# Kernel optimization log

Hardware: AMD Instinct MI355X
Metric: run time of the kernel (lower is better)

## Reference

```python
import jax, jax.numpy as jnp
import numpy as np

RATIO = 0.08  # self.ratio_3 (frozen parameter)
# kernel point k -> (dx, dy) = (k//3-1, k%3-1); matches torch.meshgrid('ij') flattening in offset_modulation
GX = np.repeat(np.arange(-1, 2), 3)  # [-1,-1,-1,0,0,0,1,1,1]
GY = np.tile(np.arange(-1, 2), 3)    # [-1,0,1,-1,0,1,-1,0,1]


def conv3(x, w, b):
    y = jax.lax.conv_general_dilated(x, w, (1, 1), ((1, 1), (1, 1)),
                                     dimension_numbers=('NCHW', 'OIHW', 'NCHW'))
    return y + b[None, :, None, None]


def offset_modulation(offset):
    B, C, H, W = offset.shape
    ov = offset.reshape(B, C // 2, 2, H, W)
    crop = ov[:, 3:12]                      # 9 (x,y) pairs
    oxy = jnp.concatenate([crop[:, :, 0], crop[:, :, 1]], axis=1) * RATIO  # [B,18,H,W]
    grid = jnp.concatenate([jnp.asarray(GX), jnp.asarray(GY)]).astype(offset.dtype)
    return oxy - grid[None, :, None, None]


def bilinear_sample(x, py, px):
    # x: [B,C,H,W]; py,px: [B,H,W] float sample coords; zero outside bounds
    B, C, H, W = x.shape
    y0 = jnp.floor(py); x0 = jnp.floor(px)
    wy = py - y0; wx = px - x0
    def gather(yi, xi):
        valid = ((yi >= 0) & (yi < H) & (xi >= 0) & (xi < W)).astype(x.dtype)
        yc = jnp.clip(yi, 0, H - 1).astype(jnp.int32)
        xc = jnp.clip(xi, 0, W - 1).astype(jnp.int32)
        g = jax.vmap(lambda img, yy, xx: img[:, yy, xx])(x, yc, xc)  # [B,C,H,W]
        return g * valid[:, None]
    return (gather(y0, x0) * ((1 - wy) * (1 - wx))[:, None]
            + gather(y0, x0 + 1) * ((1 - wy) * wx)[:, None]
            + gather(y0 + 1, x0) * (wy * (1 - wx))[:, None]
            + gather(y0 + 1, x0 + 1) * (wy * wx)[:, None])


def deform_conv(x, off, w, b):
    # off: [B,18,H,W], channels 0..8 = dx per kernel point, 9..17 = dy
    B, C, H, W = x.shape
    by = jnp.arange(H, dtype=x.dtype)[None, :, None]
    bx = jnp.arange(W, dtype=x.dtype)[None, None, :]
    out = jnp.zeros((B, w.shape[0], H, W), x.dtype)
    for k in range(9):
        py = by + GY[k] + off[:, 9 + k]
        px = bx + GX[k] + off[:, k]
        s = bilinear_sample(x, py, px)
        out = out + jnp.einsum('bchw,oc->bohw', s, w[:, :, GY[k] + 1, GX[k] + 1])
    return out + b[None, :, None, None]


def setup_inputs():
    key = jax.random.key(0)
    ks = iter(jax.random.split(key, 32))
    def p(*shape):
        return jax.random.normal(next(ks), shape, jnp.float32) * 0.05
    inp = {
        'x': jax.random.normal(next(ks), (2, 64, 256, 256), jnp.float32),
        'offset_0': jax.random.normal(next(ks), (2, 24, 256, 256), jnp.float32),
        'l12_w': p(64, 64, 3, 3), 'l12_b': p(64),
        'l13_w1': p(64, 64, 3, 3), 'l13_b1': p(64),
        'l13_w2': p(64, 64, 3, 3), 'l13_b2': p(64),
        'l14_w1': p(64, 64, 3, 3), 'l14_b1': p(64),
        'l14_w2': p(64, 64, 3, 3), 'l14_b2': p(64),
        'l15_w': p(32, 64, 3, 3), 'l15_b': p(32),
        'd50_w': p(32, 32, 3, 3), 'd50_b': p(32),
        'd51_w': p(32, 32, 3, 3), 'd51_b': p(32),
        'd60_w': p(32, 32, 3, 3), 'd60_b': p(32),
        'd61_w': p(32, 32, 3, 3), 'd61_b': p(32),
        'l24_w': p(3, 32, 3, 3), 'l24_b': p(3),
    }
    return inp


def reference(x, offset_0, l12_w, l12_b, l13_w1, l13_b1, l13_w2, l13_b2,
              l14_w1, l14_b1, l14_w2, l14_b2, l15_w, l15_b,
              d50_w, d50_b, d51_w, d51_b, d60_w, d60_b, d61_w, d61_b,
              l24_w, l24_b):
    off = offset_modulation(offset_0)
    x = conv3(x, l12_w, l12_b)
    x = conv3(jax.nn.relu(conv3(x, l13_w1, l13_b1)), l13_w2, l13_b2) + x
    x = conv3(jax.nn.relu(conv3(x, l14_w1, l14_b1)), l14_w2, l14_b2) + x
    x = conv3(x, l15_w, l15_b)
    r5 = jax.nn.relu(deform_conv(x, off, d50_w, d50_b))
    r5 = deform_conv(r5, off, d51_w, d51_b)
    x = x + r5
    r6 = jax.nn.relu(deform_conv(x, off, d60_w, d60_b))
    r6 = deform_conv(r6, off, d61_w, d61_b)
    x = x + r6
    return conv3(x, l24_w, l24_b)
```

## Files before the change

### kernel.cpp

```cpp
#include <hip/hip_runtime.h>

#define HH 256
#define WW 256
#define HW (HH * WW)

typedef float f32x4 __attribute__((ext_vector_type(4)));
typedef short bf16x8 __attribute__((ext_vector_type(8)));

__device__ __forceinline__ unsigned short f2bf(float f) {
    union { float f; unsigned u; } v; v.f = f;
    unsigned r = v.u + 0x7fff + ((v.u >> 16) & 1);
    return (unsigned short)(r >> 16);
}
__device__ __forceinline__ float bflo(unsigned u) {
    union { unsigned u; float f; } v; v.u = u << 16; return v.f;
}
__device__ __forceinline__ float bfhi(unsigned u) {
    union { unsigned u; float f; } v; v.u = u & 0xffff0000u; return v.f;
}

__global__ void prepack_all(
    const float* w0, const float* w1, const float* w2, const float* w3,
    const float* w4, const float* w5, const float* w6, const float* w7,
    const float* w8, const float* w9,
    unsigned short* d0, unsigned short* d1, unsigned short* d2,
    unsigned short* d3, unsigned short* d4, unsigned short* d5,
    unsigned short* d6, unsigned short* d7, unsigned short* d8,
    unsigned short* d9) {
    const int L = blockIdx.y;
    const float* w; unsigned short* dst; int COUT, CIN;
    switch (L) {
        case 0: w = w0; dst = d0; COUT = 64; CIN = 64; break;
        case 1: w = w1; dst = d1; COUT = 64; CIN = 64; break;
        case 2: w = w2; dst = d2; COUT = 64; CIN = 64; break;
        case 3: w = w3; dst = d3; COUT = 64; CIN = 64; break;
        case 4: w = w4; dst = d4; COUT = 64; CIN = 64; break;
        case 5: w = w5; dst = d5; COUT = 32; CIN = 64; break;
        case 6: w = w6; dst = d6; COUT = 32; CIN = 32; break;
        case 7: w = w7; dst = d7; COUT = 32; CIN = 32; break;
        case 8: w = w8; dst = d8; COUT = 32; CIN = 32; break;
        default: w = w9; dst = d9; COUT = 32; CIN = 32; break;
    }
    int n = COUT * CIN * 9;
    int i = blockIdx.x * 256 + threadIdx.x;
    if (i >= n) return;
    int q = i & 31;
    int rest = i >> 5;
    int o = rest % COUT;
    int rest2 = rest / COUT;
    int KC = CIN >> 5;
    int kc = rest2 % KC;
    int t = rest2 / KC;
    int cin = kc * 32 + q;
    float v = w[((o * CIN + cin) * 3 + t / 3) * 3 + (t % 3)];
    dst[i] = f2bf(v);
}

template <bool SRCF32, int CIN, int COUT>
__global__ __launch_bounds__((COUT / 32) * 128) void convmfma(
    const void* __restrict__ in_, const unsigned short* __restrict__ wp,
    const float* __restrict__ bias, unsigned short* __restrict__ out) {
    constexpr int KC = CIN / 32;
    constexpr int WM = COUT / 32;
    constexpr int NT = WM * 128;
    constexpr int CSTR = 72;
    __shared__ unsigned short xt[204 * CSTR];

    const int tid = threadIdx.x;
    const int b = blockIdx.z;
    const int bx0 = blockIdx.x * 32;
    const int by0 = blockIdx.y * 4;

    if (SRCF32) {
        const float* inb = (const float*)in_ + (size_t)b * CIN * HW;
        for (int hp = tid; hp < 204; hp += NT) {
            int hy = hp / 34, hx = hp - hy * 34;
            int gy = by0 + hy - 1, gx = bx0 + hx - 1;
            bool ok = ((unsigned)gy < HH) && ((unsigned)gx < WW);
            const float* src = inb + ((size_t)gy * WW + gx);
            unsigned* dstp = (unsigned*)&xt[hp * CSTR];
#pragma unroll 4
            for (int c = 0; c < CIN; c += 2) {
                float v0 = ok ? src[(size_t)c * HW] : 0.f;
                float v1 = ok ? src[(size_t)(c + 1) * HW] : 0.f;
                dstp[c >> 1] = (unsigned)f2bf(v0) | ((unsigned)f2bf(v1) << 16);
            }
        }
    } else {
        const unsigned short* inb = (const unsigned short*)in_ + (size_t)b * HW * CIN;
        constexpr int CH = CIN / 8;
        for (int idx = tid; idx < 204 * CH; idx += NT) {
            int hp = idx / CH, sub = idx - hp * CH;
            int hy = hp / 34, hx = hp - hy * 34;
            int gy = by0 + hy - 1, gx = bx0 + hx - 1;
            uint4 v = {0, 0, 0, 0};
            if (((unsigned)gy < HH) && ((unsigned)gx < WW))
                v = *(const uint4*)&inb[((size_t)gy * WW + gx) * CIN + sub * 8];
            *(uint4*)&xt[hp * CSTR + sub * 8] = v;
        }
    }
    __syncthreads();

    const int lane = tid & 63;
    const int wv = tid >> 6;
    const int wm = (WM == 2) ? (wv & 1) : 0;
    const int wn = (WM == 2) ? (wv >> 1) : wv;
    const int l15 = lane & 15;
    const int kg = lane >> 4;

    f32x4 acc[2][4];
#pragma unroll
    for (int m = 0; m < 2; ++m)
#pragma unroll
        for (int n = 0; n < 4; ++n) acc[m][n] = {0.f, 0.f, 0.f, 0.f};

    int hbase[4];
#pragma unroll
    for (int n = 0; n < 4; ++n) {
        int p = wn * 64 + n * 16 + l15;
        hbase[n] = (p >> 5) * 34 + (p & 31);
    }

    const unsigned short* wlane = wp + ((size_t)(wm * 32 + l15) * 4 + kg) * 8;

#pragma unroll
    for (int t = 0; t < 9; ++t) {
        bf16x8 afr[2][KC];
#pragma unroll
        for (int kc = 0; kc < KC; ++kc)
#pragma unroll
            for (int m = 0; m < 2; ++m)
                afr[m][kc] = *(const bf16x8*)(wlane + ((size_t)(t * KC + kc) * COUT + m * 16) * 32);

        const int hoff = (t / 3) * 34 + (t % 3);
#pragma unroll
        for (int kc = 0; kc < KC; ++kc) {
            bf16x8 bfr[4];
#pragma unroll
            for (int n = 0; n < 4; ++n)
                bfr[n] = *(const bf16x8*)&xt[(hbase[n] + hoff) * CSTR + kc * 32 + kg * 8];
#pragma unroll
            for (int m = 0; m < 2; ++m)
#pragma unroll
                for (int n = 0; n < 4; ++n)
                    acc[m][n] = __builtin_amdgcn_mfma_f32_16x16x32_bf16(afr[m][kc], bfr[n], acc[m][n], 0, 0, 0);
        }
    }

    const size_t pixbase = (size_t)b * HW;
#pragma unroll
    for (int m = 0; m < 2; ++m) {
#pragma unroll
        for (int n = 0; n < 4; ++n) {
            int p = wn * 64 + n * 16 + l15;
            int gy = by0 + (p >> 5), gx = bx0 + (p & 31);
            size_t pidx = (pixbase + (size_t)gy * WW + gx) * COUT;
            int cb = wm * 32 + m * 16 + kg * 4;
            float v[4];
#pragma unroll
            for (int r = 0; r < 4; ++r) v[r] = acc[m][n][r] + bias[cb + r];
            uint2 o;
            o.x = (unsigned)f2bf(v[0]) | ((unsigned)f2bf(v[1]) << 16);
            o.y = (unsigned)f2bf(v[2]) | ((unsigned)f2bf(v[3]) << 16);
            *(uint2*)&out[pidx + cb] = o;
        }
    }
}

__global__ __launch_bounds__(256) void fusedres(
    const unsigned short* __restrict__ in, const unsigned short* __restrict__ w1p,
    const float* __restrict__ b1, const unsigned short* __restrict__ w2p,
    const float* __restrict__ b2, unsigned short* __restrict__ out) {
    constexpr int CS = 72;
    constexpr int MIDB = 160 * CS;
    __shared__ unsigned short xt[(160 + 128) * CS];

    const int tid = threadIdx.x;
    const int b = blockIdx.z;
    const int bx0 = blockIdx.x * 16;
    const int by0 = blockIdx.y * 4;

    const unsigned short* inb = in + (size_t)b * HW * 64;
    for (int idx = tid; idx < 160 * 8; idx += 256) {
        int hp = idx >> 3, sub = idx & 7;
        int hy = hp / 20, hx = hp - hy * 20;
        int gy = by0 + hy - 2, gx = bx0 + hx - 2;
        uint4 v = {0, 0, 0, 0};
        if (((unsigned)gy < HH) && ((unsigned)gx < WW))
            v = *(const uint4*)&inb[((size_t)gy * WW + gx) * 64 + sub * 8];
        *(uint4*)&xt[hp * CS + sub * 8] = v;
    }
    __syncthreads();

    const int lane = tid & 63;
    const int wv = tid >> 6;
    const int l15 = lane & 15;
    const int kg = lane >> 4;
    const int wm = wv & 1;
    const int gh = wv >> 1;

    f32x4 acc1[2][4];
#pragma unroll
    for (int m = 0; m < 2; ++m)
#pragma unroll
        for (int n = 0; n < 4; ++n) acc1[m][n] = {0.f, 0.f, 0.f, 0.f};

    int ib[4];
#pragma unroll
    for (int n = 0; n < 4; ++n) {
        int id = gh * 64 + n * 16 + l15;
        int rid = min(id, 107);
        int iy = rid / 18, ix = rid - iy * 18;
        ib[n] = iy * 20 + ix;
    }

    const unsigned short* w1l = w1p + ((size_t)(wm * 32 + l15) * 4 + kg) * 8;
#pragma unroll
    for (int t = 0; t < 9; ++t) {
        bf16x8 afr[2][2];
#pragma unroll
        for (int kc = 0; kc < 2; ++kc)
#pragma unroll
            for (int m = 0; m < 2; ++m)
                afr[kc][m] = *(const bf16x8*)(w1l + ((size_t)(t * 2 + kc) * 64 + m * 16) * 32);
        const int hoff = (t / 3) * 20 + (t % 3);
#pragma unroll
        for (int kc = 0; kc < 2; ++kc) {
            bf16x8 bfr[4];
#pragma unroll
            for (int n = 0; n < 4; ++n)
                bfr[n] = *(const bf16x8*)&xt[(ib[n] + hoff) * CS + kc * 32 + kg * 8];
#pragma unroll
            for (int m = 0; m < 2; ++m)
#pragma unroll
                for (int n = 0; n < 4; ++n)
                    acc1[m][n] = __builtin_amdgcn_mfma_f32_16x16x32_bf16(afr[kc][m], bfr[n], acc1[m][n], 0, 0, 0);
        }
    }
#pragma unroll
    for (int n = 0; n < 4; ++n) {
        int id = gh * 64 + n * 16 + l15;
        int rid = min(id, 107);
        int iy = rid / 18, ix = rid - iy * 18;
        int gy = by0 - 1 + iy, gx = bx0 - 1 + ix;
        bool ok = ((unsigned)gy < HH) && ((unsigned)gx < WW) && (id < 108);
#pragma unroll
        for (int m = 0; m < 2; ++m) {
            int cb = wm * 32 + m * 16 + kg * 4;
            float v[4];
#pragma unroll
            for (int r = 0; r < 4; ++r)
                v[r] = ok ? fmaxf(acc1[m][n][r] + b1[cb + r], 0.f) : 0.f;
            uint2 o;
            o.x = (unsigned)f2bf(v[0]) | ((unsigned)f2bf(v[1]) << 16);
            o.y = (unsigned)f2bf(v[2]) | ((unsigned)f2bf(v[3]) << 16);
            *(uint2*)&xt[MIDB + id * CS + cb] = o;
        }
    }
    __syncthreads();

    f32x4 acc2[2][2];
#pragma unroll
    for (int m = 0; m < 2; ++m)
#pragma unroll
        for (int n = 0; n < 2; ++n) acc2[m][n] = {0.f, 0.f, 0.f, 0.f};

    int mb[2];
#pragma unroll
    for (int n = 0; n < 2; ++n) {
        int p = gh * 32 + n * 16 + l15;
        mb[n] = (p >> 4) * 18 + (p & 15);
    }
    const unsigned short* w2l = w2p + ((size_t)(wm * 32 + l15) * 4 + kg) * 8;
#pragma unroll
    for (int t = 0; t < 9; ++t) {
        bf16x8 afr[2][2];
#pragma unroll
        for (int kc = 0; kc < 2; ++kc)
#pragma unroll
            for (int m = 0; m < 2; ++m)
                afr[kc][m] = *(const bf16x8*)(w2l + ((size_t)(t * 2 + kc) * 64 + m * 16) * 32);
        const int hoff = (t / 3) * 18 + (t % 3);
#pragma unroll
        for (int kc = 0; kc < 2; ++kc) {
            bf16x8 bfr[2];
#pragma unroll
            for (int n = 0; n < 2; ++n)
                bfr[n] = *(const bf16x8*)&xt[MIDB + (mb[n] + hoff) * CS + kc * 32 + kg * 8];
#pragma unroll
            for (int m = 0; m < 2; ++m)
#pragma unroll
                for (int n = 0; n < 2; ++n)
                    acc2[m][n] = __builtin_amdgcn_mfma_f32_16x16x32_bf16(afr[kc][m], bfr[n], acc2[m][n], 0, 0, 0);
        }
    }

    unsigned short* outb = out + (size_t)b * HW * 64;
#pragma unroll
    for (int n = 0; n < 2; ++n) {
        int p = gh * 32 + n * 16 + l15;
        int oy = p >> 4, ox = p & 15;
        int gy = by0 + oy, gx = bx0 + ox;
        int rs = (oy + 2) * 20 + ox + 2;
        size_t pidx = ((size_t)gy * WW + gx) * 64;
#pragma unroll
        for (int m = 0; m < 2; ++m) {
            int cb = wm * 32 + m * 16 + kg * 4;
            float v[4];
#pragma unroll
            for (int r = 0; r < 4; ++r) v[r] = acc2[m][n][r] + b2[cb + r];
            uint2 rr = *(const uint2*)&xt[rs * CS + cb];
            v[0] += bflo(rr.x); v[1] += bfhi(rr.x);
            v[2] += bflo(rr.y); v[3] += bfhi(rr.y);
            uint2 o;
            o.x = (unsigned)f2bf(v[0]) | ((unsigned)f2bf(v[1]) << 16);
            o.y = (unsigned)f2bf(v[2]) | ((unsigned)f2bf(v[3]) << 16);
            *(uint2*)&outb[pidx + cb] = o;
        }
    }
}

__global__ __launch_bounds__(512) void dpair(
    const unsigned short* __restrict__ in, const float* __restrict__ off0,
    const unsigned short* __restrict__ w1p, const float* __restrict__ b1,
    const unsigned short* __restrict__ w2p, const float* __restrict__ b2,
    unsigned short* __restrict__ out) {
    constexpr int CS = 40;
    constexpr int MIDB = 432 * CS;
    __shared__ unsigned short xt[(432 + 352) * CS];

    const int tid = threadIdx.x;
    const int b = blockIdx.z;
    const int bx0 = blockIdx.x * 32;
    const int by0 = blockIdx.y * 8;

    const unsigned short* inb = in + (size_t)b * HW * 32;
    for (int idx = tid; idx < 432 * 4; idx += 512) {
        int hp = idx >> 2, sub = idx & 3;
        int hy = hp / 36, hx = hp - hy * 36;
        int gy = by0 + hy - 2, gx = bx0 + hx - 2;
        uint4 v = {0, 0, 0, 0};
        if (((unsigned)gy < HH) && ((unsigned)gx < WW))
            v = *(const uint4*)&inb[((size_t)gy * WW + gx) * 32 + sub * 8];
        *(uint4*)&xt[hp * CS + sub * 8] = v;
    }
    __syncthreads();

    const int lane = tid & 63;
    const int wv = tid >> 6;
    const int l15 = lane & 15;
    const int kg = lane >> 4;
    const float* offB = off0 + (size_t)b * 24 * HW;

    f32x4 acc1[2][3];
#pragma unroll
    for (int m = 0; m < 2; ++m)
#pragma unroll
        for (int f = 0; f < 3; ++f) acc1[m][f] = {0.f, 0.f, 0.f, 0.f};

    int fgy[3], fgx[3], foff[3];
#pragma unroll
    for (int f = 0; f < 3; ++f) {
        int id = (wv * 3 + f) * 16 + l15;
        int rid = min(id, 339);
        int iy = rid / 34, ix = rid - iy * 34;
        fgy[f] = by0 - 1 + iy;
        fgx[f] = bx0 - 1 + ix;
        int cy = min(max(fgy[f], 0), HH - 1);
        int cx = min(max(fgx[f], 0), WW - 1);
        foff[f] = cy * WW + cx;
    }
    const unsigned short* w1l = w1p + (size_t)(l15 * 32 + kg * 8);

#pragma unroll 1
    for (int t = 0; t < 9; ++t) {
        const int k = (t % 3) * 3 + t / 3;
        const float* offx = offB + (size_t)(6 + 2 * k) * HW;
        const float* offy = offB + (size_t)(7 + 2 * k) * HW;
        bf16x8 afr[2];
#pragma unroll
        for (int m = 0; m < 2; ++m)
            afr[m] = *(const bf16x8*)(w1l + (size_t)(t * 32 + m * 16) * 32);

        bf16x8 bfr[3];
#pragma unroll
        for (int f = 0; f < 3; ++f) {
            float dxv = offx[foff[f]] * 0.08f;
            float dyv = offy[foff[f]] * 0.08f;
            float pxf = (float)fgx[f] + dxv;
            float pyf = (float)fgy[f] + dyv;
            float x0f = floorf(pxf), y0f = floorf(pyf);
            float wx = pxf - x0f, wy = pyf - y0f;
            int tx0 = min(max((int)x0f - (bx0 - 2), 0), 34);
            int ty0 = min(max((int)y0f - (by0 - 2), 0), 10);
            int lp = ty0 * 36 + tx0;
            uint4 a00 = *(const uint4*)&xt[lp * CS + kg * 8];
            uint4 a01 = *(const uint4*)&xt[(lp + 1) * CS + kg * 8];
            uint4 a10 = *(const uint4*)&xt[(lp + 36) * CS + kg * 8];
            uint4 a11 = *(const uint4*)&xt[(lp + 37) * CS + kg * 8];
            float w00 = (1.f - wy) * (1.f - wx), w01 = (1.f - wy) * wx;
            float w10 = wy * (1.f - wx), w11 = wy * wx;
            unsigned c00[4] = {a00.x, a00.y, a00.z, a00.w};
            unsigned c01[4] = {a01.x, a01.y, a01.z, a01.w};
            unsigned c10[4] = {a10.x, a10.y, a10.z, a10.w};
            unsigned c11[4] = {a11.x, a11.y, a11.z, a11.w};
            union { bf16x8 v; unsigned u[4]; } ur;
#pragma unroll
            for (int j = 0; j < 4; ++j) {
                float slo = w00 * bflo(c00[j]) + w01 * bflo(c01[j]) +
                            w10 * bflo(c10[j]) + w11 * bflo(c11[j]);
                float shi = w00 * bfhi(c00[j]) + w01 * bfhi(c01[j]) +
                            w10 * bfhi(c10[j]) + w11 * bfhi(c11[j]);
                ur.u[j] = (unsigned)f2bf(slo) | ((unsigned)f2bf(shi) << 16);
            }
            bfr[f] = ur.v;
        }
#pragma unroll
        for (int m = 0; m < 2; ++m)
#pragma unroll
            for (int f = 0; f < 3; ++f)
                acc1[m][f] = __builtin_amdgcn_mfma_f32_16x16x32_bf16(afr[m], bfr[f], acc1[m][f], 0, 0, 0);
    }
#pragma unroll
    for (int f = 0; f < 3; ++f) {
        int id = (wv * 3 + f) * 16 + l15;
        bool ok = ((unsigned)fgy[f] < HH) && ((unsigned)fgx[f] < WW) && (id < 340);
        int wid = min(id, 351);
#pragma unroll
        for (int m = 0; m < 2; ++m) {
            int cb = m * 16 + kg * 4;
            float v[4];
#pragma unroll
            for (int r = 0; r < 4; ++r)
                v[r] = ok ? fmaxf(acc1[m][f][r] + b1[cb + r], 0.f) : 0.f;
            uint2 o;
            o.x = (unsigned)f2bf(v[0]) | ((unsigned)f2bf(v[1]) << 16);
            o.y = (unsigned)f2bf(v[2]) | ((unsigned)f2bf(v[3]) << 16);
            *(uint2*)&xt[MIDB + wid * CS + cb] = o;
        }
    }
    __syncthreads();

    f32x4 acc2[2][2];
#pragma unroll
    for (int m = 0; m < 2; ++m)
#pragma unroll
        for (int n = 0; n < 2; ++n) acc2[m][n] = {0.f, 0.f, 0.f, 0.f};

    const int py = by0 + wv;
    const unsigned short* w2l = w2p + (size_t)(l15 * 32 + kg * 8);

#pragma unroll 1
    for (int t = 0; t < 9; ++t) {
        const int k = (t % 3) * 3 + t / 3;
        const float* offx = offB + (size_t)(6 + 2 * k) * HW + (size_t)py * WW;
        const float* offy = offB + (size_t)(7 + 2 * k) * HW + (size_t)py * WW;
        bf16x8 afr[2];
#pragma unroll
        for (int m = 0; m < 2; ++m)
            afr[m] = *(const bf16x8*)(w2l + (size_t)(t * 32 + m * 16) * 32);

        bf16x8 bfr[2];
#pragma unroll
        for (int n = 0; n < 2; ++n) {
            const int pxi = bx0 + n * 16 + l15;
            float dxv = offx[pxi] * 0.08f;
            float dyv = offy[pxi] * 0.08f;
            float pxf = (float)pxi + dxv;
            float pyf = (float)py + dyv;
            float x0f = floorf(pxf), y0f = floorf(pyf);
            float wx = pxf - x0f, wy = pyf - y0f;
            int mx0 = min(max((int)x0f - (bx0 - 1), 0), 32);
            int my0 = min(max((int)y0f - (by0 - 1), 0), 8);
            int lp = my0 * 34 + mx0;
            uint4 a00 = *(const uint4*)&xt[MIDB + lp * CS + kg * 8];
            uint4 a01 = *(const uint4*)&xt[MIDB + (lp + 1) * CS + kg * 8];
            uint4 a10 = *(const uint4*)&xt[MIDB + (lp + 34) * CS + kg * 8];
            uint4 a11 = *(const uint4*)&xt[MIDB + (lp + 35) * CS + kg * 8];
            float w00 = (1.f - wy) * (1.f - wx), w01 = (1.f - wy) * wx;
            float w10 = wy * (1.f - wx), w11 = wy * wx;
            unsigned c00[4] = {a00.x, a00.y, a00.z, a00.w};
            unsigned c01[4] = {a01.x, a01.y, a01.z, a01.w};
            unsigned c10[4] = {a10.x, a10.y, a10.z, a10.w};
            unsigned c11[4] = {a11.x, a11.y, a11.z, a11.w};
            union { bf16x8 v; unsigned u[4]; } ur;
#pragma unroll
            for (int j = 0; j < 4; ++j) {
                float slo = w00 * bflo(c00[j]) + w01 * bflo(c01[j]) +
                            w10 * bflo(c10[j]) + w11 * bflo(c11[j]);
                float shi = w00 * bfhi(c00[j]) + w01 * bfhi(c01[j]) +
                            w10 * bfhi(c10[j]) + w11 * bfhi(c11[j]);
                ur.u[j] = (unsigned)f2bf(slo) | ((unsigned)f2bf(shi) << 16);
            }
            bfr[n] = ur.v;
        }
#pragma unroll
        for (int m = 0; m < 2; ++m)
#pragma unroll
            for (int n = 0; n < 2; ++n)
                acc2[m][n] = __builtin_amdgcn_mfma_f32_16x16x32_bf16(afr[m], bfr[n], acc2[m][n], 0, 0, 0);
    }

    unsigned short* outb = out + (size_t)b * HW * 32;
#pragma unroll
    for (int n = 0; n < 2; ++n) {
        int gx = bx0 + n * 16 + l15;
        int rs = (wv + 2) * 36 + (n * 16 + l15) + 2;
        size_t pidx = ((size_t)py * WW + gx) * 32;
#pragma unroll
        for (int m = 0; m < 2; ++m) {
            int cb = m * 16 + kg * 4;
            float v[4];
#pragma unroll
            for (int r = 0; r < 4; ++r) v[r] = acc2[m][n][r] + b2[cb + r];
            uint2 rr = *(const uint2*)&xt[rs * CS + cb];
            v[0] += bflo(rr.x); v[1] += bfhi(rr.x);
            v[2] += bflo(rr.y); v[3] += bfhi(rr.y);
            uint2 o;
            o.x = (unsigned)f2bf(v[0]) | ((unsigned)f2bf(v[1]) << 16);
            o.y = (unsigned)f2bf(v[2]) | ((unsigned)f2bf(v[3]) << 16);
            *(uint2*)&outb[pidx + cb] = o;
        }
    }
}

__global__ __launch_bounds__(256) void conv3f(const unsigned short* __restrict__ in,
                                              const float* __restrict__ wgt,
                                              const float* __restrict__ bias,
                                              float* __restrict__ out) {
    __shared__ unsigned short xt[324 * 34];
    const int tid = threadIdx.x;
    const int lx = tid & 15, ly = tid >> 4;
    const int bx = blockIdx.x << 4, by = blockIdx.y << 4;
    const int b = blockIdx.z;

    const unsigned short* inb = in + (size_t)b * HW * 32;
    for (int idx = tid; idx < 324 * 8; idx += 256) {
        int hp = idx >> 3, sub = idx & 7;
        int hy = hp / 18, hx = hp - hy * 18;
        int gy = by + hy - 1, gx = bx + hx - 1;
        uint2 v = {0, 0};
        if (((unsigned)gy < HH) && ((unsigned)gx < WW))
            v = *(const uint2*)&inb[((size_t)gy * WW + gx) * 32 + sub * 4];
        *(uint2*)&xt[hp * 34 + sub * 4] = v;
    }
    __syncthreads();

    float a0 = bias[0], a1 = bias[1], a2 = bias[2];
#pragma unroll
    for (int ty = 0; ty < 3; ++ty) {
#pragma unroll
        for (int tx = 0; tx < 3; ++tx) {
            const unsigned short* row = &xt[((ly + ty) * 18 + lx + tx) * 34];
#pragma unroll 8
            for (int c = 0; c < 32; c += 2) {
                unsigned pv = *(const unsigned*)&row[c];
                float vl = bflo(pv), vh = bfhi(pv);
                const float* wl = wgt + (size_t)(c * 3 + ty) * 3 + tx;
                const float* whp = wgt + (size_t)((c + 1) * 3 + ty) * 3 + tx;
                a0 = fmaf(vl, wl[0], a0);          a0 = fmaf(vh, whp[0], a0);
                a1 = fmaf(vl, wl[32 * 9], a1);     a1 = fmaf(vh, whp[32 * 9], a1);
                a2 = fmaf(vl, wl[64 * 9], a2);     a2 = fmaf(vh, whp[64 * 9], a2);
            }
        }
    }
    const size_t o0 = ((size_t)b * 3) * HW + (size_t)(by + ly) * WW + bx + lx;
    out[o0] = a0;
    out[o0 + HW] = a1;
    out[o0 + 2 * HW] = a2;
}

extern "C" void kernel_launch(void* const* d_in, const int* in_sizes, int n_in,
                              void* d_out, int out_size, void* d_ws, size_t ws_size,
                              hipStream_t stream) {
    const float* x    = (const float*)d_in[0];
    const float* off0 = (const float*)d_in[1];
    const float* w12  = (const float*)d_in[2];
    const float* b12  = (const float*)d_in[3];
    const float* w13a = (const float*)d_in[4];
    const float* b13a = (const float*)d_in[5];
    const float* w13b = (const float*)d_in[6];
    const float* b13b = (const float*)d_in[7];
    const float* w14a = (const float*)d_in[8];
    const float* b14a = (const float*)d_in[9];
    const float* w14b = (const float*)d_in[10];
    const float* b14b = (const float*)d_in[11];
    const float* w15  = (const float*)d_in[12];
    const float* b15  = (const float*)d_in[13];
    const float* w50  = (const float*)d_in[14];
    const float* b50  = (const float*)d_in[15];
    const float* w51  = (const float*)d_in[16];
    const float* b51  = (const float*)d_in[17];
    const float* w60  = (const float*)d_in[18];
    const float* b60  = (const float*)d_in[19];
    const float* w61  = (const float*)d_in[20];
    const float* b61  = (const float*)d_in[21];
    const float* w24  = (const float*)d_in[22];
    const float* b24  = (const float*)d_in[23];

    unsigned short* A  = (unsigned short*)d_ws;
    unsigned short* Bb = A + (size_t)2 * HW * 64;
    unsigned short* D  = Bb;
    unsigned short* E  = Bb + (size_t)2 * HW * 32;
    unsigned short* wpk = Bb + (size_t)2 * HW * 64;
    const int SZ64 = 64 * 64 * 9;
    const int SZ32 = 32 * 64 * 9;
    const int SZD  = 32 * 32 * 9;
    unsigned short* p12  = wpk;
    unsigned short* p13a = p12 + SZ64;
    unsigned short* p13b = p13a + SZ64;
    unsigned short* p14a = p13b + SZ64;
    unsigned short* p14b = p14a + SZ64;
    unsigned short* p15  = p14b + SZ64;
    unsigned short* q50  = p15 + SZ32;
    unsigned short* q51  = q50 + SZD;
    unsigned short* q60  = q51 + SZD;
    unsigned short* q61  = q60 + SZD;
    float* out = (float*)d_out;

    prepack_all<<<dim3(144, 10), 256, 0, stream>>>(
        w12, w13a, w13b, w14a, w14b, w15, w50, w51, w60, w61,
        p12, p13a, p13b, p14a, p14b, p15, q50, q51, q60, q61);

    dim3 gm(WW / 32, HH / 4, 2);
    dim3 gf(WW / 16, HH / 4, 2);
    dim3 gd(WW / 32, HH / 8, 2);
    dim3 gs(HH / 16, WW / 16, 2);

    convmfma<true, 64, 64><<<gm, 256, 0, stream>>>(x, p12, b12, A);
    fusedres<<<gf, 256, 0, stream>>>(A,  p13a, b13a, p13b, b13b, Bb);
    fusedres<<<gf, 256, 0, stream>>>(Bb, p14a, b14a, p14b, b14b, A);
    convmfma<false, 64, 32><<<gm, 128, 0, stream>>>(A, p15, b15, D);
    dpair<<<gd, 512, 0, stream>>>(D, off0, q50, b50, q51, b51, E);
    dpair<<<gd, 512, 0, stream>>>(E, off0, q60, b60, q61, b61, D);
    conv3f<<<gs, 256, 0, stream>>>(D, w24, b24, out);
}
```

Before: 251.5 us.

## Replace fused residual-block kernels with separate larger-tile conv launches

Removes the fusedres kernel, which computed both convs of each residual block with a recomputed halo for the intermediate. Each residual block now runs as two convmfma launches with ReLU and residual-add epilogue template flags. convmfma is retiled so each 256-thread block covers an 8x32 pixel tile and each wave computes all output channels for its 2 rows, which increases weight reuse per block. The change removes the halo recompute but adds an extra round trip of the intermediate activation through global memory and two more launches. It also reads and writes A in place in the residual step, which is safe only because each pixel is read and written by the same thread.

```diff
diff --git a/kernel.cpp b/kernel.cpp
--- a/kernel.cpp
+++ b/kernel.cpp
@@ -56,24 +56,24 @@
     dst[i] = f2bf(v);
 }
 
-template <bool SRCF32, int CIN, int COUT>
-__global__ __launch_bounds__((COUT / 32) * 128) void convmfma(
+template <bool SRCF32, int CIN, int COUT, bool RELU, bool ADDRES>
+__global__ __launch_bounds__(256) void convmfma(
     const void* __restrict__ in_, const unsigned short* __restrict__ wp,
-    const float* __restrict__ bias, unsigned short* __restrict__ out) {
+    const float* __restrict__ bias, const unsigned short* __restrict__ res,
+    unsigned short* __restrict__ out) {
     constexpr int KC = CIN / 32;
-    constexpr int WM = COUT / 32;
-    constexpr int NT = WM * 128;
+    constexpr int WM = COUT / 16;
     constexpr int CSTR = 72;
-    __shared__ unsigned short xt[204 * CSTR];
+    __shared__ unsigned short xt[340 * CSTR];
 
     const int tid = threadIdx.x;
     const int b = blockIdx.z;
     const int bx0 = blockIdx.x * 32;
-    const int by0 = blockIdx.y * 4;
+    const int by0 = blockIdx.y * 8;
 
     if (SRCF32) {
         const float* inb = (const float*)in_ + (size_t)b * CIN * HW;
-        for (int hp = tid; hp < 204; hp += NT) {
+        for (int hp = tid; hp < 340; hp += 256) {
             int hy = hp / 34, hx = hp - hy * 34;
             int gy = by0 + hy - 1, gx = bx0 + hx - 1;
             bool ok = ((unsigned)gy < HH) && ((unsigned)gx < WW);
@@ -89,7 +89,7 @@
     } else {
         const unsigned short* inb = (const unsigned short*)in_ + (size_t)b * HW * CIN;
         constexpr int CH = CIN / 8;
-        for (int idx = tid; idx < 204 * CH; idx += NT) {
+        for (int idx = tid; idx < 340 * CH; idx += 256) {
             int hp = idx / CH, sub = idx - hp * CH;
             int hy = hp / 34, hx = hp - hy * 34;
             int gy = by0 + hy - 1, gx = bx0 + hx - 1;
@@ -103,33 +103,31 @@
 
     const int lane = tid & 63;
     const int wv = tid >> 6;
-    const int wm = (WM == 2) ? (wv & 1) : 0;
-    const int wn = (WM == 2) ? (wv >> 1) : wv;
     const int l15 = lane & 15;
     const int kg = lane >> 4;
 
-    f32x4 acc[2][4];
-#pragma unroll
-    for (int m = 0; m < 2; ++m)
+    f32x4 acc[WM][4];
+#pragma unroll
+    for (int m = 0; m < WM; ++m)
 #pragma unroll
         for (int n = 0; n < 4; ++n) acc[m][n] = {0.f, 0.f, 0.f, 0.f};
 
     int hbase[4];
 #pragma unroll
     for (int n = 0; n < 4; ++n) {
-        int p = wn * 64 + n * 16 + l15;
-        hbase[n] = (p >> 5) * 34 + (p & 31);
-    }
-
-    const unsigned short* wlane = wp + ((size_t)(wm * 32 + l15) * 4 + kg) * 8;
+        int p = n * 16 + l15;
+        hbase[n] = (2 * wv + (p >> 5)) * 34 + (p & 31);
+    }
+
+    const unsigned short* wlane = wp + ((size_t)l15 * 4 + kg) * 8;
 
 #pragma unroll
     for (int t = 0; t < 9; ++t) {
-        bf16x8 afr[2][KC];
+        bf16x8 afr[WM][KC];
 #pragma unroll
         for (int kc = 0; kc < KC; ++kc)
 #pragma unroll
-            for (int m = 0; m < 2; ++m)
+            for (int m = 0; m < WM; ++m)
                 afr[m][kc] = *(const bf16x8*)(wlane + ((size_t)(t * KC + kc) * COUT + m * 16) * 32);
 
         const int hoff = (t / 3) * 34 + (t % 3);
@@ -140,7 +138,7 @@
             for (int n = 0; n < 4; ++n)
                 bfr[n] = *(const bf16x8*)&xt[(hbase[n] + hoff) * CSTR + kc * 32 + kg * 8];
 #pragma unroll
-            for (int m = 0; m < 2; ++m)
+            for (int m = 0; m < WM; ++m)
 #pragma unroll
                 for (int n = 0; n < 4; ++n)
                     acc[m][n] = __builtin_amdgcn_mfma_f32_16x16x32_bf16(afr[m][kc], bfr[n], acc[m][n], 0, 0, 0);
@@ -149,173 +147,28 @@
 
     const size_t pixbase = (size_t)b * HW;
 #pragma unroll
-    for (int m = 0; m < 2; ++m) {
-#pragma unroll
-        for (int n = 0; n < 4; ++n) {
-            int p = wn * 64 + n * 16 + l15;
-            int gy = by0 + (p >> 5), gx = bx0 + (p & 31);
-            size_t pidx = (pixbase + (size_t)gy * WW + gx) * COUT;
-            int cb = wm * 32 + m * 16 + kg * 4;
+    for (int n = 0; n < 4; ++n) {
+        int p = n * 16 + l15;
+        int gy = by0 + 2 * wv + (p >> 5), gx = bx0 + (p & 31);
+        size_t pidx = (pixbase + (size_t)gy * WW + gx) * COUT;
+#pragma unroll
+        for (int m = 0; m < WM; ++m) {
+            int cb = m * 16 + kg * 4;
             float v[4];
 #pragma unroll
-            for (int r = 0; r < 4; ++r) v[r] = acc[m][n][r] + bias[cb + r];
+            for (int r = 0; r < 4; ++r) {
+                v[r] = acc[m][n][r] + bias[cb + r];
+                if (RELU) v[r] = fmaxf(v[r], 0.f);
+            }
+            if (ADDRES) {
+                uint2 rr = *(const uint2*)&res[pidx + cb];
+                v[0] += bflo(rr.x); v[1] += bfhi(rr.x);
+                v[2] += bflo(rr.y); v[3] += bfhi(rr.y);
+            }
             uint2 o;
             o.x = (unsigned)f2bf(v[0]) | ((unsigned)f2bf(v[1]) << 16);
             o.y = (unsigned)f2bf(v[2]) | ((unsigned)f2bf(v[3]) << 16);
             *(uint2*)&out[pidx + cb] = o;
-        }
-    }
-}
-
-__global__ __launch_bounds__(256) void fusedres(
-    const unsigned short* __restrict__ in, const unsigned short* __restrict__ w1p,
-    const float* __restrict__ b1, const unsigned short* __restrict__ w2p,
-    const float* __restrict__ b2, unsigned short* __restrict__ out) {
-    constexpr int CS = 72;
-    constexpr int MIDB = 160 * CS;
-    __shared__ unsigned short xt[(160 + 128) * CS];
-
-    const int tid = threadIdx.x;
-    const int b = blockIdx.z;
-    const int bx0 = blockIdx.x * 16;
-    const int by0 = blockIdx.y * 4;
-
-    const unsigned short* inb = in + (size_t)b * HW * 64;
-    for (int idx = tid; idx < 160 * 8; idx += 256) {
-        int hp = idx >> 3, sub = idx & 7;
-        int hy = hp / 20, hx = hp - hy * 20;
-        int gy = by0 + hy - 2, gx = bx0 + hx - 2;
-        uint4 v = {0, 0, 0, 0};
-        if (((unsigned)gy < HH) && ((unsigned)gx < WW))
-            v = *(const uint4*)&inb[((size_t)gy * WW + gx) * 64 + sub * 8];
-        *(uint4*)&xt[hp * CS + sub * 8] = v;
-    }
-    __syncthreads();
-
-    const int lane = tid & 63;
-    const int wv = tid >> 6;
-    const int l15 = lane & 15;
-    const int kg = lane >> 4;
-    const int wm = wv & 1;
-    const int gh = wv >> 1;
-
-    f32x4 acc1[2][4];
-#pragma unroll
-    for (int m = 0; m < 2; ++m)
-#pragma unroll
-        for (int n = 0; n < 4; ++n) acc1[m][n] = {0.f, 0.f, 0.f, 0.f};
-
-    int ib[4];
-#pragma unroll
-    for (int n = 0; n < 4; ++n) {
-        int id = gh * 64 + n * 16 + l15;
-        int rid = min(id, 107);
-        int iy = rid / 18, ix = rid - iy * 18;
-        ib[n] = iy * 20 + ix;
-    }
-
-    const unsigned short* w1l = w1p + ((size_t)(wm * 32 + l15) * 4 + kg) * 8;
-#pragma unroll
-    for (int t = 0; t < 9; ++t) {
-        bf16x8 afr[2][2];
-#pragma unroll
-        for (int kc = 0; kc < 2; ++kc)
-#pragma unroll
-            for (int m = 0; m < 2; ++m)
-                afr[kc][m] = *(const bf16x8*)(w1l + ((size_t)(t * 2 + kc) * 64 + m * 16) * 32);
-        const int hoff = (t / 3) * 20 + (t % 3);
-#pragma unroll
-        for (int kc = 0; kc < 2; ++kc) {
-            bf16x8 bfr[4];
-#pragma unroll
-            for (int n = 0; n < 4; ++n)
-                bfr[n] = *(const bf16x8*)&xt[(ib[n] + hoff) * CS + kc * 32 + kg * 8];
-#pragma unroll
-            for (int m = 0; m < 2; ++m)
-#pragma unroll
-                for (int n = 0; n < 4; ++n)
-                    acc1[m][n] = __builtin_amdgcn_mfma_f32_16x16x32_bf16(afr[kc][m], bfr[n], acc1[m][n], 0, 0, 0);
-        }
-    }
-#pragma unroll
-    for (int n = 0; n < 4; ++n) {
-        int id = gh * 64 + n * 16 + l15;
-        int rid = min(id, 107);
-        int iy = rid / 18, ix = rid - iy * 18;
-        int gy = by0 - 1 + iy, gx = bx0 - 1 + ix;
-        bool ok = ((unsigned)gy < HH) && ((unsigned)gx < WW) && (id < 108);
-#pragma unroll
-        for (int m = 0; m < 2; ++m) {
-            int cb = wm * 32 + m * 16 + kg * 4;
-            float v[4];
-#pragma unroll
-            for (int r = 0; r < 4; ++r)
-                v[r] = ok ? fmaxf(acc1[m][n][r] + b1[cb + r], 0.f) : 0.f;
-            uint2 o;
-            o.x = (unsigned)f2bf(v[0]) | ((unsigned)f2bf(v[1]) << 16);
-            o.y = (unsigned)f2bf(v[2]) | ((unsigned)f2bf(v[3]) << 16);
-            *(uint2*)&xt[MIDB + id * CS + cb] = o;
-        }
-    }
-    __syncthreads();
-
-    f32x4 acc2[2][2];
-#pragma unroll
-    for (int m = 0; m < 2; ++m)
-#pragma unroll
-        for (int n = 0; n < 2; ++n) acc2[m][n] = {0.f, 0.f, 0.f, 0.f};
-
-    int mb[2];
-#pragma unroll
-    for (int n = 0; n < 2; ++n) {
-        int p = gh * 32 + n * 16 + l15;
-        mb[n] = (p >> 4) * 18 + (p & 15);
-    }
-    const unsigned short* w2l = w2p + ((size_t)(wm * 32 + l15) * 4 + kg) * 8;
-#pragma unroll
-    for (int t = 0; t < 9; ++t) {
-        bf16x8 afr[2][2];
-#pragma unroll
-        for (int kc = 0; kc < 2; ++kc)
-#pragma unroll
-            for (int m = 0; m < 2; ++m)
-                afr[kc][m] = *(const bf16x8*)(w2l + ((size_t)(t * 2 + kc) * 64 + m * 16) * 32);
-        const int hoff = (t / 3) * 18 + (t % 3);
-#pragma unroll
-        for (int kc = 0; kc < 2; ++kc) {
-            bf16x8 bfr[2];
-#pragma unroll
-            for (int n = 0; n < 2; ++n)
-                bfr[n] = *(const bf16x8*)&xt[MIDB + (mb[n] + hoff) * CS + kc * 32 + kg * 8];
-#pragma unroll
-            for (int m = 0; m < 2; ++m)
-#pragma unroll
-                for (int n = 0; n < 2; ++n)
-                    acc2[m][n] = __builtin_amdgcn_mfma_f32_16x16x32_bf16(afr[kc][m], bfr[n], acc2[m][n], 0, 0, 0);
-        }
-    }
-
-    unsigned short* outb = out + (size_t)b * HW * 64;
-#pragma unroll
-    for (int n = 0; n < 2; ++n) {
-        int p = gh * 32 + n * 16 + l15;
-        int oy = p >> 4, ox = p & 15;
-        int gy = by0 + oy, gx = bx0 + ox;
-        int rs = (oy + 2) * 20 + ox + 2;
-        size_t pidx = ((size_t)gy * WW + gx) * 64;
-#pragma unroll
-        for (int m = 0; m < 2; ++m) {
-            int cb = wm * 32 + m * 16 + kg * 4;
-            float v[4];
-#pragma unroll
-            for (int r = 0; r < 4; ++r) v[r] = acc2[m][n][r] + b2[cb + r];
-            uint2 rr = *(const uint2*)&xt[rs * CS + cb];
-            v[0] += bflo(rr.x); v[1] += bfhi(rr.x);
-            v[2] += bflo(rr.y); v[3] += bfhi(rr.y);
-            uint2 o;
-            o.x = (unsigned)f2bf(v[0]) | ((unsigned)f2bf(v[1]) << 16);
-            o.y = (unsigned)f2bf(v[2]) | ((unsigned)f2bf(v[3]) << 16);
-            *(uint2*)&outb[pidx + cb] = o;
         }
     }
 }
@@ -622,15 +475,17 @@
         w12, w13a, w13b, w14a, w14b, w15, w50, w51, w60, w61,
         p12, p13a, p13b, p14a, p14b, p15, q50, q51, q60, q61);
 
-    dim3 gm(WW / 32, HH / 4, 2);
-    dim3 gf(WW / 16, HH / 4, 2);
+    dim3 gm(WW / 32, HH / 8, 2);
     dim3 gd(WW / 32, HH / 8, 2);
     dim3 gs(HH / 16, WW / 16, 2);
 
-    convmfma<true, 64, 64><<<gm, 256, 0, stream>>>(x, p12, b12, A);
-    fusedres<<<gf, 256, 0, stream>>>(A,  p13a, b13a, p13b, b13b, Bb);
-    fusedres<<<gf, 256, 0, stream>>>(Bb, p14a, b14a, p14b, b14b, A);
-    convmfma<false, 64, 32><<<gm, 128, 0, stream>>>(A, p15, b15, D);
+    convmfma<true,  64, 64, false, false><<<gm, 256, 0, stream>>>(x,  p12,  b12,  nullptr, A);
+    convmfma<false, 64, 64, true,  false><<<gm, 256, 0, stream>>>(A,  p13a, b13a, nullptr, Bb);
+    convmfma<false, 64, 64, false, true ><<<gm, 256, 0, stream>>>(Bb, p13b, b13b, A, A);
+    convmfma<false, 64, 64, true,  false><<<gm, 256, 0, stream>>>(A,  p14a, b14a, nullptr, Bb);
+    convmfma<false, 64, 64, false, true ><<<gm, 256, 0, stream>>>(Bb, p14b, b14b, A, A);
+    convmfma<false, 64, 32, false, false><<<gm, 256, 0, stream>>>(A,  p15,  b15,  nullptr, D);
+
     dpair<<<gd, 512, 0, stream>>>(D, off0, q50, b50, q51, b51, E);
     dpair<<<gd, 512, 0, stream>>>(E, off0, q60, b60, q61, b61, D);
     conv3f<<<gs, 256, 0, stream>>>(D, w24, b24, out);
```

Result: no change. 254.6 us (+1.2%).
